# Kernel optimization log

Hardware: AMD Instinct MI355X
Metric: run time of the kernel (lower is better)

## Reference

```python
import jax, jax.numpy as jnp
import numpy as np

N = 50000          # num nodes
E = 800000         # edges per adjacency (avg degree 16)
NFEAT = 512
NHID = 256
NCLS = 100
LN_EPS = 1e-5


def spmm(rows, cols, vals, feat):
    # sparse [N,N] @ dense [N,F] via gather + segment-sum scatter
    return jax.ops.segment_sum(vals[:, None] * feat[cols], rows, num_segments=N)


def layernorm(h, g, b):
    mu = jnp.mean(h, axis=-1, keepdims=True)
    var = jnp.var(h, axis=-1, keepdims=True)
    return (h - mu) * jax.lax.rsqrt(var + LN_EPS) * g + b


def setup_inputs() -> dict:
    key = jax.random.key(0)
    ks = jax.random.split(key, 20)
    inp = {
        "x": jax.random.normal(ks[0], (N, NFEAT), dtype=jnp.float32),
        "adj_rows": jax.random.randint(ks[1], (4, E), 0, N, dtype=jnp.int32),
        "adj_cols": jax.random.randint(ks[2], (4, E), 0, N, dtype=jnp.int32),
        "adj_vals": jax.random.uniform(ks[3], (4, E), dtype=jnp.float32) / 16.0,
    }
    def lin(k, fin, fout):
        s = 1.0 / np.sqrt(fin)
        kw, kb = jax.random.split(k)
        return (jax.random.uniform(kw, (fin, fout), minval=-s, maxval=s, dtype=jnp.float32),
                jax.random.uniform(kb, (fout,), minval=-s, maxval=s, dtype=jnp.float32))
    # layer 0: GraphSage(nfeat -> nhid), LayerNorm over 2*nhid
    inp["W0"], inp["b0"] = lin(ks[4], NFEAT, NHID)
    inp["ln0_g"] = jnp.ones((2 * NHID,), jnp.float32)
    inp["ln0_b"] = jnp.zeros((2 * NHID,), jnp.float32)
    # layer 1: GCN(2*nhid -> nhid)
    inp["W1"], inp["b1"] = lin(ks[5], 2 * NHID, NHID)
    # layer 2: GraphSage(nhid -> nhid), LayerNorm over 2*nhid
    inp["W2"], inp["b2"] = lin(ks[6], NHID, NHID)
    inp["ln2_g"] = jnp.ones((2 * NHID,), jnp.float32)
    inp["ln2_b"] = jnp.zeros((2 * NHID,), jnp.float32)
    # layer 3: GCN(2*nhid -> nhid)
    inp["W3"], inp["b3"] = lin(ks[7], 2 * NHID, NHID)
    # output linear (nhid -> num_classes)
    inp["Wout"], inp["bout"] = lin(ks[8], NHID, NCLS)
    return inp


def reference(x, adj_rows, adj_cols, adj_vals,
              W0, b0, ln0_g, ln0_b, W1, b1, W2, b2, ln2_g, ln2_b, W3, b3,
              Wout, bout):
    # layer 0: GraphSage — feat = Linear(x); h = LN(concat([feat, A@feat])); ReLU; dropout(p=0)=id
    feat = x @ W0 + b0
    agg = spmm(adj_rows[0], adj_cols[0], adj_vals[0], feat)
    h = jax.nn.relu(layernorm(jnp.concatenate([feat, agg], axis=1), ln0_g, ln0_b))
    # layer 1: GCN — h = A @ Linear(h); ReLU
    h = jax.nn.relu(spmm(adj_rows[1], adj_cols[1], adj_vals[1], h @ W1 + b1))
    # layer 2: GraphSage
    feat = h @ W2 + b2
    agg = spmm(adj_rows[2], adj_cols[2], adj_vals[2], feat)
    h = jax.nn.relu(layernorm(jnp.concatenate([feat, agg], axis=1), ln2_g, ln2_b))
    # layer 3: GCN
    h = jax.nn.relu(spmm(adj_rows[3], adj_cols[3], adj_vals[3], h @ W3 + b3))
    # output head
    return h @ Wout + bout
```

## Files before the change

kernel.cpp:

```cpp
#include <hip/hip_runtime.h>

#define N_NODES 50000
#define E_EDGES 800000
#define NFEAT   512
#define NHID    256
#define NCLS    100
#define LN_EPS  1e-5f

#define NB     196
#define CHUNKA 6144
#define CAPB   6656

#define WT_TOTAL  (256*512 + 256*512 + 256*256 + 256*512 + 128*256)
#define XC_TOTAL  (N_NODES * NFEAT / 8)
#define PREP_TOTAL (WT_TOTAL + XC_TOTAL + 4 * NB)

typedef __attribute__((ext_vector_type(8))) short bf16x8;
typedef __attribute__((ext_vector_type(4))) float f32x4;

__device__ __forceinline__ ushort bf16_rne(float x) {
    unsigned u = __float_as_uint(x);
    unsigned r = u + 0x7FFFu + ((u >> 16) & 1u);
    return (ushort)(r >> 16);
}
__device__ __forceinline__ float bf16_to_f(ushort h) {
    return __uint_as_float(((unsigned)h) << 16);
}

__device__ __forceinline__ void gload16(const void* g, void* l) {
    __builtin_amdgcn_global_load_lds(
        (const __attribute__((address_space(1))) unsigned int*)g,
        (__attribute__((address_space(3))) unsigned int*)l, 16, 0, 0);
}

__global__ __launch_bounds__(256)
void prep_kernel(const float* __restrict__ W0, const float* __restrict__ W1,
                 const float* __restrict__ W2, const float* __restrict__ W3,
                 const float* __restrict__ Wo, const float* __restrict__ x,
                 ushort* __restrict__ W0T, ushort* __restrict__ W1T,
                 ushort* __restrict__ W2T, ushort* __restrict__ W3T,
                 ushort* __restrict__ WoT, ushort* __restrict__ Xb,
                 int* __restrict__ bcur)
{
    int idx = blockIdx.x * 256 + threadIdx.x;
    if (idx < WT_TOTAL) {
        const float* W; ushort* WT; int K, Nc;
        if      (idx < 131072) { W = W0; WT = W0T; K = 512; Nc = 256; }
        else if (idx < 262144) { idx -= 131072; W = W1; WT = W1T; K = 512; Nc = 256; }
        else if (idx < 327680) { idx -= 262144; W = W2; WT = W2T; K = 256; Nc = 256; }
        else if (idx < 458752) { idx -= 327680; W = W3; WT = W3T; K = 512; Nc = 256; }
        else                   { idx -= 458752; W = Wo; WT = WoT; K = 256; Nc = 100; }
        const int n = idx / K, k = idx - n * K;
        WT[idx] = bf16_rne((n < Nc) ? W[(size_t)k * Nc + n] : 0.f);
        return;
    }
    idx -= WT_TOTAL;
    if (idx < XC_TOTAL) {
        const float4 v0 = ((const float4*)x)[idx * 2];
        const float4 v1 = ((const float4*)x)[idx * 2 + 1];
        bf16x8 h;
        h[0] = (short)bf16_rne(v0.x); h[1] = (short)bf16_rne(v0.y);
        h[2] = (short)bf16_rne(v0.z); h[3] = (short)bf16_rne(v0.w);
        h[4] = (short)bf16_rne(v1.x); h[5] = (short)bf16_rne(v1.y);
        h[6] = (short)bf16_rne(v1.z); h[7] = (short)bf16_rne(v1.w);
        *(bf16x8*)&Xb[idx * 8] = h;
        return;
    }
    idx -= XC_TOTAL;
    if (idx < 4 * NB) bcur[idx] = 0;
}

template<int SWZ, int WF32, int WBF>
__global__ __launch_bounds__(512)
void gemm_mfma_bf16(const ushort* __restrict__ A1, const ushort* __restrict__ A2,
                    int K1, int K, const ushort* __restrict__ BT,
                    const float* __restrict__ bias, float* __restrict__ C,
                    ushort* __restrict__ Cbf, int M, int Nc)
{
    __shared__ __align__(16) ushort Ah[2][128 * 32];
    __shared__ __align__(16) ushort Bh[2][128 * 32];

    int bx, by;
    if (SWZ) {
        const int bid = blockIdx.x;
        const int g = bid >> 4;
        const int r = bid & 15;
        bx = g * 8 + (r & 7);
        by = r >> 3;
        if (bx >= (M + 127) / 128) return;
    } else {
        bx = blockIdx.x;
        by = blockIdx.y;
    }

    const int tid = threadIdx.x;
    const int bm  = bx * 128;
    const int bn  = by * 128;
    const int w   = tid >> 6;
    const int l   = tid & 63;
    const int wm  = (w >> 2) * 64;
    const int wn  = (w & 3) * 32;
    const int fr  = l & 15;
    const int fq  = l >> 4;

    const int gro = l >> 2;
    const int gch = ((l & 3) ^ (gro & 3)) * 8;
    const int ldsbase = (16 * w) * 32;

    f32x4 acc[4][2];
    #pragma unroll
    for (int i = 0; i < 4; ++i) {
        acc[i][0] = (f32x4){0.f, 0.f, 0.f, 0.f};
        acc[i][1] = (f32x4){0.f, 0.f, 0.f, 0.f};
    }

    const int K2 = K - K1;
    const int NS = K / 32;

    auto stage = [&](int s, int b) {
        const int k0 = s * 32;
        gload16(&BT[(size_t)(bn + 16 * w + gro) * K + k0 + gch], &Bh[b][ldsbase]);
        const ushort* asrc;
        if (k0 < K1) asrc = &A1[(size_t)(bm + 16 * w + gro) * K1 + k0 + gch];
        else         asrc = &A2[(size_t)(bm + 16 * w + gro) * K2 + (k0 - K1) + gch];
        gload16(asrc, &Ah[b][ldsbase]);
    };

    stage(0, 0);
    __syncthreads();

    int cur = 0;
    for (int s = 0; s < NS; ++s) {
        if (s + 1 < NS) stage(s + 1, cur ^ 1);

        bf16x8 bf[2];
        #pragma unroll
        for (int nf = 0; nf < 2; ++nf) {
            const int r = wn + nf * 16 + fr;
            bf[nf] = *(const bf16x8*)&Bh[cur][r * 32 + ((fq ^ (r & 3)) * 8)];
        }
        #pragma unroll
        for (int mf = 0; mf < 4; ++mf) {
            const int r = wm + mf * 16 + fr;
            const bf16x8 af = *(const bf16x8*)&Ah[cur][r * 32 + ((fq ^ (r & 3)) * 8)];
            acc[mf][0] = __builtin_amdgcn_mfma_f32_16x16x32_bf16(af, bf[0], acc[mf][0], 0, 0, 0);
            acc[mf][1] = __builtin_amdgcn_mfma_f32_16x16x32_bf16(af, bf[1], acc[mf][1], 0, 0, 0);
        }
        __syncthreads();
        cur ^= 1;
    }

    #pragma unroll
    for (int mf = 0; mf < 4; ++mf) {
        #pragma unroll
        for (int r = 0; r < 4; ++r) {
            const int row = bm + wm + mf * 16 + fq * 4 + r;
            if (row >= M) continue;
            #pragma unroll
            for (int nf = 0; nf < 2; ++nf) {
                const int col = bn + wn + nf * 16 + fr;
                if (col < Nc) {
                    const float v = acc[mf][nf][r] + bias[col];
                    if (WF32) C[(size_t)row * Nc + col] = v;
                    if (WBF)  Cbf[(size_t)row * Nc + col] = bf16_rne(v);
                }
            }
        }
    }
}

__global__ __launch_bounds__(256)
void bin_kernel(const int* __restrict__ rows, const int* __restrict__ cols,
                const float* __restrict__ vals, int* __restrict__ bcur,
                int2* __restrict__ est)
{
    __shared__ int cnt[NB];
    __shared__ int scn[256];
    __shared__ int cstart[NB];
    __shared__ int ccur[NB];
    __shared__ int garr[NB];
    __shared__ __align__(16) int2 buf[CHUNKA];

    const int a  = blockIdx.y;
    const int e0 = blockIdx.x * CHUNKA;
    const int n  = min(CHUNKA, E_EDGES - e0);
    const int t  = threadIdx.x;
    const int*   rp = rows + (size_t)a * E_EDGES + e0;
    const int*   cp = cols + (size_t)a * E_EDGES + e0;
    const float* vp = vals + (size_t)a * E_EDGES + e0;

    if (t < NB) cnt[t] = 0;
    __syncthreads();
    for (int i = t; i < n; i += 256) atomicAdd(&cnt[((unsigned)rp[i]) >> 8], 1);
    __syncthreads();

    scn[t] = (t < NB) ? cnt[t] : 0;
    __syncthreads();
    for (int off = 1; off < 256; off <<= 1) {
        const int v = (t >= off) ? scn[t - off] : 0;
        __syncthreads();
        scn[t] += v;
        __syncthreads();
    }
    if (t < NB) {
        const int ex = scn[t] - cnt[t];
        cstart[t] = ex;
        ccur[t]   = ex;
        garr[t]   = atomicAdd(&bcur[a * NB + t], cnt[t]);
    }
    __syncthreads();

    for (int i = t; i < n; i += 256) {
        const unsigned r = (unsigned)rp[i];
        const int b = r >> 8;
        const int p = atomicAdd(&ccur[b], 1);
        buf[p] = make_int2((int)((r << 16) | (unsigned)cp[i]), __float_as_int(vp[i]));
    }
    __syncthreads();

    for (int i = t; i < n; i += 256) {
        const int2 en = buf[i];
        const int b = ((unsigned)en.x) >> 24;
        const int slot = garr[b] + (i - cstart[b]);
        if (slot < CAPB)
            est[((size_t)(a * NB + b)) * CAPB + slot] = en;
    }
}

__global__ __launch_bounds__(256)
void sort_kernel(const int* __restrict__ bcur, const int2* __restrict__ est,
                 int2* __restrict__ cpk, int* __restrict__ rowstart)
{
    __shared__ __align__(16) int2 sbuf[CAPB];
    __shared__ __align__(16) int2 obuf[CAPB];
    __shared__ int cnt[256];
    __shared__ int scn[256];
    __shared__ int cur[256];

    const int a = blockIdx.y;
    const int b = blockIdx.x;
    const int t = threadIdx.x;
    const int nb = min(bcur[a * NB + b], CAPB);
    const int2* ei = est + ((size_t)(a * NB + b)) * CAPB;

    scn[t] = (t < b) ? bcur[a * NB + t] : 0;
    __syncthreads();
    for (int o = 128; o > 0; o >>= 1) {
        if (t < o) scn[t] += scn[t + o];
        __syncthreads();
    }
    const int bb = scn[0];
    __syncthreads();

    for (int i = t; i < nb; i += 256) sbuf[i] = ei[i];
    cnt[t] = 0;
    __syncthreads();
    for (int i = t; i < nb; i += 256)
        atomicAdd(&cnt[(((unsigned)sbuf[i].x) >> 16) & 255], 1);
    __syncthreads();

    scn[t] = cnt[t];
    __syncthreads();
    for (int off = 1; off < 256; off <<= 1) {
        const int v = (t >= off) ? scn[t - off] : 0;
        __syncthreads();
        scn[t] += v;
        __syncthreads();
    }
    const int excl = scn[t] - cnt[t];
    cur[t] = excl;

    const int r0 = b << 8;
    if (r0 + t < N_NODES)
        rowstart[(size_t)a * (N_NODES + 1) + r0 + t] = bb + excl;
    if (b == NB - 1 && t == 0)
        rowstart[(size_t)a * (N_NODES + 1) + N_NODES] = E_EDGES;
    __syncthreads();

    for (int i = t; i < nb; i += 256) {
        const int2 en = sbuf[i];
        const int r = (((unsigned)en.x) >> 16) & 255;
        const int p = atomicAdd(&cur[r], 1);
        obuf[p] = make_int2(en.x & 0xFFFF, en.y);
    }
    __syncthreads();

    int2* co = cpk + (size_t)a * E_EDGES + bb;
    for (int i = t; i < nb; i += 256) co[i] = obuf[i];
}

template<int LNFUSE>
__global__ __launch_bounds__(256)
void spmm_kernel(const int* __restrict__ rowstart, const int2* __restrict__ cpk,
                 const ushort* __restrict__ feat, ushort* __restrict__ out0,
                 ushort* __restrict__ out1, const float* __restrict__ g,
                 const float* __restrict__ be)
{
    const int row  = __builtin_amdgcn_readfirstlane((blockIdx.x * 256 + threadIdx.x) >> 6);
    const int lane = threadIdx.x & 63;

    const int s = __builtin_amdgcn_readfirstlane(rowstart[row]);
    const int e = __builtin_amdgcn_readfirstlane(rowstart[row + 1]);

    const ushort* fbase = feat + lane * 4;
    float ax = 0.f, ay = 0.f, az = 0.f, aw = 0.f;

    int j = s;
    for (; j + 16 <= e; j += 16) {
        #pragma unroll
        for (int q = 0; q < 16; ++q) {
            const int2 ev = cpk[j + q];
            const float v = __int_as_float(ev.y);
            const uint2 f = *(const uint2*)(fbase + (size_t)ev.x * NHID);
            ax += v * __uint_as_float(f.x << 16);
            ay += v * __uint_as_float(f.x & 0xFFFF0000u);
            az += v * __uint_as_float(f.y << 16);
            aw += v * __uint_as_float(f.y & 0xFFFF0000u);
        }
    }
    for (; j < e; ++j) {
        const int2 ev = cpk[j];
        const float v = __int_as_float(ev.y);
        const uint2 f = *(const uint2*)(fbase + (size_t)ev.x * NHID);
        ax += v * __uint_as_float(f.x << 16);
        ay += v * __uint_as_float(f.x & 0xFFFF0000u);
        az += v * __uint_as_float(f.y << 16);
        aw += v * __uint_as_float(f.y & 0xFFFF0000u);
    }

    if (LNFUSE) {
        const uint2 fx = *(const uint2*)(fbase + (size_t)row * NHID);
        float xf[4] = {__uint_as_float(fx.x << 16), __uint_as_float(fx.x & 0xFFFF0000u),
                       __uint_as_float(fx.y << 16), __uint_as_float(fx.y & 0xFFFF0000u)};

        float sum = xf[0] + xf[1] + xf[2] + xf[3] + ax + ay + az + aw;
        #pragma unroll
        for (int m = 1; m < 64; m <<= 1) sum += __shfl_xor(sum, m, 64);
        const float mean = sum * (1.f / 512.f);

        float sq = 0.f;
        #pragma unroll
        for (int jj = 0; jj < 4; ++jj) { const float d = xf[jj] - mean; sq += d * d; }
        { float d; d = ax - mean; sq += d * d; d = ay - mean; sq += d * d;
          d = az - mean; sq += d * d; d = aw - mean; sq += d * d; }
        #pragma unroll
        for (int m = 1; m < 64; m <<= 1) sq += __shfl_xor(sq, m, 64);
        const float rstd = rsqrtf(sq * (1.f / 512.f) + LN_EPS);

        const int col = lane * 4;
        const float av[4] = {ax, ay, az, aw};
        ushort4 o0, o1;
        float t0[4], t1[4];
        #pragma unroll
        for (int jj = 0; jj < 4; ++jj) {
            t0[jj] = fmaxf((xf[jj] - mean) * rstd * g[col + jj] + be[col + jj], 0.f);
            t1[jj] = fmaxf((av[jj] - mean) * rstd * g[256 + col + jj] + be[256 + col + jj], 0.f);
        }
        o0.x = bf16_rne(t0[0]); o0.y = bf16_rne(t0[1]); o0.z = bf16_rne(t0[2]); o0.w = bf16_rne(t0[3]);
        o1.x = bf16_rne(t1[0]); o1.y = bf16_rne(t1[1]); o1.z = bf16_rne(t1[2]); o1.w = bf16_rne(t1[3]);
        *(ushort4*)&out0[(size_t)row * NHID + col] = o0;
        *(ushort4*)&out1[(size_t)row * NHID + col] = o1;
    } else {
        ushort4 o;
        o.x = bf16_rne(fmaxf(ax, 0.f)); o.y = bf16_rne(fmaxf(ay, 0.f));
        o.z = bf16_rne(fmaxf(az, 0.f)); o.w = bf16_rne(fmaxf(aw, 0.f));
        *(ushort4*)&out0[(size_t)row * NHID + lane * 4] = o;
    }
}

extern "C" void kernel_launch(void* const* d_in, const int* in_sizes, int n_in,
                              void* d_out, int out_size, void* d_ws, size_t ws_size,
                              hipStream_t stream)
{
    const float* x    = (const float*)d_in[0];
    const int*   rows = (const int*)  d_in[1];
    const int*   cols = (const int*)  d_in[2];
    const float* vals = (const float*)d_in[3];
    const float* W0   = (const float*)d_in[4];
    const float* b0   = (const float*)d_in[5];
    const float* g0   = (const float*)d_in[6];
    const float* be0  = (const float*)d_in[7];
    const float* W1   = (const float*)d_in[8];
    const float* b1   = (const float*)d_in[9];
    const float* W2   = (const float*)d_in[10];
    const float* b2   = (const float*)d_in[11];
    const float* g2   = (const float*)d_in[12];
    const float* be2  = (const float*)d_in[13];
    const float* W3   = (const float*)d_in[14];
    const float* b3   = (const float*)d_in[15];
    const float* Wout = (const float*)d_in[16];
    const float* bout = (const float*)d_in[17];
    float* out = (float*)d_out;

    char* wsb = (char*)d_ws;
    size_t off = 0;
    auto carve = [&](size_t bytes) { void* p = wsb + off; off += (bytes + 255) & ~(size_t)255; return p; };
    int*    rowstart = (int*)   carve((size_t)4 * (N_NODES + 1) * 4);
    int*    bcur     = (int*)   carve((size_t)4 * NB * 4);
    int2*   cpk      = (int2*)  carve((size_t)4 * E_EDGES * 8);
    int2*   est      = (int2*)  carve((size_t)4 * NB * CAPB * 8);
    ushort* Xb       = (ushort*)carve((size_t)N_NODES * NFEAT * 2);
    ushort* F        = (ushort*)carve((size_t)N_NODES * NHID * 2);
    ushort* P        = (ushort*)carve((size_t)N_NODES * NHID * 2);
    ushort* Q        = (ushort*)carve((size_t)N_NODES * NHID * 2);
    ushort* G        = (ushort*)carve((size_t)N_NODES * NHID * 2);
    ushort* H        = (ushort*)carve((size_t)N_NODES * NHID * 2);
    ushort* W0T = (ushort*)carve((size_t)256 * 512 * 2);
    ushort* W1T = (ushort*)carve((size_t)256 * 512 * 2);
    ushort* W2T = (ushort*)carve((size_t)256 * 256 * 2);
    ushort* W3T = (ushort*)carve((size_t)256 * 512 * 2);
    ushort* WoT = (ushort*)carve((size_t)128 * 256 * 2);
    carve(131072);

    const dim3 blk(256);
    const dim3 blkg(512);
    const dim3 g_gemm(784);
    const dim3 g_head(391, 1);
    const dim3 g_bin((E_EDGES + CHUNKA - 1) / CHUNKA, 4);
    const dim3 g_sort(NB, 4);
    const int  row_blocks  = (N_NODES * 64 + 255) / 256;
    const int  prep_blocks = (PREP_TOTAL + 255) / 256;

    prep_kernel<<<prep_blocks, blk, 0, stream>>>(W0, W1, W2, W3, Wout, x,
                                                 W0T, W1T, W2T, W3T, WoT, Xb, bcur);
    bin_kernel<<<g_bin, blk, 0, stream>>>(rows, cols, vals, bcur, est);
    sort_kernel<<<g_sort, blk, 0, stream>>>(bcur, est, cpk, rowstart);

    const int* rs0 = rowstart;
    const int* rs1 = rowstart + (N_NODES + 1);
    const int* rs2 = rowstart + 2 * (N_NODES + 1);
    const int* rs3 = rowstart + 3 * (N_NODES + 1);
    const int2* c0 = cpk;
    const int2* c1 = cpk + E_EDGES;
    const int2* c2 = cpk + 2 * (size_t)E_EDGES;
    const int2* c3 = cpk + 3 * (size_t)E_EDGES;

    gemm_mfma_bf16<1,0,1><<<g_gemm, blkg, 0, stream>>>(Xb, Xb, 512, 512, W0T, b0, nullptr, F, N_NODES, 256);
    spmm_kernel<1><<<row_blocks, blk, 0, stream>>>(rs0, c0, F, P, Q, g0, be0);

    gemm_mfma_bf16<1,0,1><<<g_gemm, blkg, 0, stream>>>(P, Q, 256, 512, W1T, b1, nullptr, G, N_NODES, 256);
    spmm_kernel<0><<<row_blocks, blk, 0, stream>>>(rs1, c1, G, H, nullptr, nullptr, nullptr);

    gemm_mfma_bf16<1,0,1><<<g_gemm, blkg, 0, stream>>>(H, H, 256, 256, W2T, b2, nullptr, F, N_NODES, 256);
    spmm_kernel<1><<<row_blocks, blk, 0, stream>>>(rs2, c2, F, P, Q, g2, be2);

    gemm_mfma_bf16<1,0,1><<<g_gemm, blkg, 0, stream>>>(P, Q, 256, 512, W3T, b3, nullptr, G, N_NODES, 256);
    spmm_kernel<0><<<row_blocks, blk, 0, stream>>>(rs3, c3, G, H, nullptr, nullptr, nullptr);

    gemm_mfma_bf16<0,1,0><<<g_head, blkg, 0, stream>>>(H, H, 256, 256, WoT, bout, out, nullptr, N_NODES, 100);
}
```

Measured before the change: 471.2 us.

## Split SpMM into column-sliced row-group kernel and separate LayerNorm pass

Replaces the one-wave-per-row SpMM with a column-sliced kernel. Each 8-lane group handles one row for a 32-column slice, and eight slice blocks cover the 256 columns. The goal is more parallelism and smaller per-edge gathers that may fit cache behaviour better. The LayerNorm and ReLU that were fused into the SpMM epilogue move to a separate ln_pair_bf16 kernel. This adds an extra write and read of the aggregated features, re-reads the edge lists eight times, puts rows of different degree inside one wave, and drops the 16-way unrolled gather loop.

```diff
diff --git a/kernel.cpp b/kernel.cpp
--- a/kernel.cpp
+++ b/kernel.cpp
@@ -289,83 +289,93 @@
     for (int i = t; i < nb; i += 256) co[i] = obuf[i];
 }
 
-template<int LNFUSE>
+template<int RELU>
 __global__ __launch_bounds__(256)
-void spmm_kernel(const int* __restrict__ rowstart, const int2* __restrict__ cpk,
-                 const ushort* __restrict__ feat, ushort* __restrict__ out0,
-                 ushort* __restrict__ out1, const float* __restrict__ g,
-                 const float* __restrict__ be)
-{
-    const int row  = __builtin_amdgcn_readfirstlane((blockIdx.x * 256 + threadIdx.x) >> 6);
-    const int lane = threadIdx.x & 63;
-
-    const int s = __builtin_amdgcn_readfirstlane(rowstart[row]);
-    const int e = __builtin_amdgcn_readfirstlane(rowstart[row + 1]);
-
-    const ushort* fbase = feat + lane * 4;
+void spmm_slice(const int* __restrict__ rowstart, const int2* __restrict__ cpk,
+                const ushort* __restrict__ feat, ushort* __restrict__ out)
+{
+    const int bid   = blockIdx.x;
+    const int slice = bid & 7;
+    const int rblk  = bid >> 3;
+    const int t     = threadIdx.x;
+    const int w     = t >> 6;
+    const int lane  = t & 63;
+    const int grp   = lane >> 3;
+    const int l8    = lane & 7;
+
+    const int row = rblk * 32 + w * 8 + grp;
+    if (row >= N_NODES) return;
+
+    const int s = rowstart[row];
+    const int e = rowstart[row + 1];
+
+    const ushort* fb = feat + slice * 32 + l8 * 4;
     float ax = 0.f, ay = 0.f, az = 0.f, aw = 0.f;
 
-    int j = s;
-    for (; j + 16 <= e; j += 16) {
-        #pragma unroll
-        for (int q = 0; q < 16; ++q) {
-            const int2 ev = cpk[j + q];
-            const float v = __int_as_float(ev.y);
-            const uint2 f = *(const uint2*)(fbase + (size_t)ev.x * NHID);
-            ax += v * __uint_as_float(f.x << 16);
-            ay += v * __uint_as_float(f.x & 0xFFFF0000u);
-            az += v * __uint_as_float(f.y << 16);
-            aw += v * __uint_as_float(f.y & 0xFFFF0000u);
-        }
-    }
-    for (; j < e; ++j) {
+    for (int j = s; j < e; ++j) {
         const int2 ev = cpk[j];
         const float v = __int_as_float(ev.y);
-        const uint2 f = *(const uint2*)(fbase + (size_t)ev.x * NHID);
+        const uint2 f = *(const uint2*)(fb + (size_t)ev.x * NHID);
         ax += v * __uint_as_float(f.x << 16);
         ay += v * __uint_as_float(f.x & 0xFFFF0000u);
         az += v * __uint_as_float(f.y << 16);
         aw += v * __uint_as_float(f.y & 0xFFFF0000u);
     }
 
-    if (LNFUSE) {
-        const uint2 fx = *(const uint2*)(fbase + (size_t)row * NHID);
-        float xf[4] = {__uint_as_float(fx.x << 16), __uint_as_float(fx.x & 0xFFFF0000u),
-                       __uint_as_float(fx.y << 16), __uint_as_float(fx.y & 0xFFFF0000u)};
-
-        float sum = xf[0] + xf[1] + xf[2] + xf[3] + ax + ay + az + aw;
-        #pragma unroll
-        for (int m = 1; m < 64; m <<= 1) sum += __shfl_xor(sum, m, 64);
-        const float mean = sum * (1.f / 512.f);
-
-        float sq = 0.f;
-        #pragma unroll
-        for (int jj = 0; jj < 4; ++jj) { const float d = xf[jj] - mean; sq += d * d; }
-        { float d; d = ax - mean; sq += d * d; d = ay - mean; sq += d * d;
-          d = az - mean; sq += d * d; d = aw - mean; sq += d * d; }
-        #pragma unroll
-        for (int m = 1; m < 64; m <<= 1) sq += __shfl_xor(sq, m, 64);
-        const float rstd = rsqrtf(sq * (1.f / 512.f) + LN_EPS);
-
-        const int col = lane * 4;
-        const float av[4] = {ax, ay, az, aw};
-        ushort4 o0, o1;
-        float t0[4], t1[4];
-        #pragma unroll
-        for (int jj = 0; jj < 4; ++jj) {
-            t0[jj] = fmaxf((xf[jj] - mean) * rstd * g[col + jj] + be[col + jj], 0.f);
-            t1[jj] = fmaxf((av[jj] - mean) * rstd * g[256 + col + jj] + be[256 + col + jj], 0.f);
-        }
-        o0.x = bf16_rne(t0[0]); o0.y = bf16_rne(t0[1]); o0.z = bf16_rne(t0[2]); o0.w = bf16_rne(t0[3]);
-        o1.x = bf16_rne(t1[0]); o1.y = bf16_rne(t1[1]); o1.z = bf16_rne(t1[2]); o1.w = bf16_rne(t1[3]);
-        *(ushort4*)&out0[(size_t)row * NHID + col] = o0;
-        *(ushort4*)&out1[(size_t)row * NHID + col] = o1;
-    } else {
-        ushort4 o;
-        o.x = bf16_rne(fmaxf(ax, 0.f)); o.y = bf16_rne(fmaxf(ay, 0.f));
-        o.z = bf16_rne(fmaxf(az, 0.f)); o.w = bf16_rne(fmaxf(aw, 0.f));
-        *(ushort4*)&out0[(size_t)row * NHID + lane * 4] = o;
-    }
+    if (RELU) {
+        ax = fmaxf(ax, 0.f); ay = fmaxf(ay, 0.f);
+        az = fmaxf(az, 0.f); aw = fmaxf(aw, 0.f);
+    }
+    ushort4 o;
+    o.x = bf16_rne(ax); o.y = bf16_rne(ay);
+    o.z = bf16_rne(az); o.w = bf16_rne(aw);
+    *(ushort4*)&out[(size_t)row * NHID + slice * 32 + l8 * 4] = o;
+}
+
+__global__ __launch_bounds__(256)
+void ln_pair_bf16(const ushort* __restrict__ F, const ushort* __restrict__ AGG,
+                  const float* __restrict__ g, const float* __restrict__ be,
+                  ushort* __restrict__ P, ushort* __restrict__ Q)
+{
+    const int gid  = blockIdx.x * 256 + threadIdx.x;
+    const int row  = gid >> 6;
+    const int lane = gid & 63;
+    if (row >= N_NODES) return;
+
+    const ushort* src = (lane < 32) ? &F[(size_t)row * NHID + lane * 8]
+                                    : &AGG[(size_t)row * NHID + (lane - 32) * 8];
+    ushort* dst = (lane < 32) ? &P[(size_t)row * NHID + lane * 8]
+                              : &Q[(size_t)row * NHID + (lane - 32) * 8];
+
+    const ushort4 a0 = ((const ushort4*)src)[0];
+    const ushort4 a1 = ((const ushort4*)src)[1];
+    float x[8] = {bf16_to_f(a0.x), bf16_to_f(a0.y), bf16_to_f(a0.z), bf16_to_f(a0.w),
+                  bf16_to_f(a1.x), bf16_to_f(a1.y), bf16_to_f(a1.z), bf16_to_f(a1.w)};
+
+    float s = 0.f;
+    #pragma unroll
+    for (int j = 0; j < 8; ++j) s += x[j];
+    #pragma unroll
+    for (int m = 1; m < 64; m <<= 1) s += __shfl_xor(s, m, 64);
+    const float mean = s * (1.f / 512.f);
+
+    float sq = 0.f;
+    #pragma unroll
+    for (int j = 0; j < 8; ++j) { const float d = x[j] - mean; sq += d * d; }
+    #pragma unroll
+    for (int m = 1; m < 64; m <<= 1) sq += __shfl_xor(sq, m, 64);
+    const float rstd = rsqrtf(sq * (1.f / 512.f) + LN_EPS);
+
+    const int fb = lane * 8;
+    float o[8];
+    #pragma unroll
+    for (int j = 0; j < 8; ++j)
+        o[j] = fmaxf((x[j] - mean) * rstd * g[fb + j] + be[fb + j], 0.f);
+    ushort4 o0, o1;
+    o0.x = bf16_rne(o[0]); o0.y = bf16_rne(o[1]); o0.z = bf16_rne(o[2]); o0.w = bf16_rne(o[3]);
+    o1.x = bf16_rne(o[4]); o1.y = bf16_rne(o[5]); o1.z = bf16_rne(o[6]); o1.w = bf16_rne(o[7]);
+    ((ushort4*)dst)[0] = o0;
+    ((ushort4*)dst)[1] = o1;
 }
 
 extern "C" void kernel_launch(void* const* d_in, const int* in_sizes, int n_in,
@@ -418,6 +428,7 @@
     const dim3 g_head(391, 1);
     const dim3 g_bin((E_EDGES + CHUNKA - 1) / CHUNKA, 4);
     const dim3 g_sort(NB, 4);
+    const dim3 g_spmm(((N_NODES + 31) / 32) * 8);
     const int  row_blocks  = (N_NODES * 64 + 255) / 256;
     const int  prep_blocks = (PREP_TOTAL + 255) / 256;
 
@@ -436,16 +447,18 @@
     const int2* c3 = cpk + 3 * (size_t)E_EDGES;
 
     gemm_mfma_bf16<1,0,1><<<g_gemm, blkg, 0, stream>>>(Xb, Xb, 512, 512, W0T, b0, nullptr, F, N_NODES, 256);
-    spmm_kernel<1><<<row_blocks, blk, 0, stream>>>(rs0, c0, F, P, Q, g0, be0);
+    spmm_slice<0><<<g_spmm, blk, 0, stream>>>(rs0, c0, F, G);
+    ln_pair_bf16<<<row_blocks, blk, 0, stream>>>(F, G, g0, be0, P, Q);
 
     gemm_mfma_bf16<1,0,1><<<g_gemm, blkg, 0, stream>>>(P, Q, 256, 512, W1T, b1, nullptr, G, N_NODES, 256);
-    spmm_kernel<0><<<row_blocks, blk, 0, stream>>>(rs1, c1, G, H, nullptr, nullptr, nullptr);
+    spmm_slice<1><<<g_spmm, blk, 0, stream>>>(rs1, c1, G, H);
 
     gemm_mfma_bf16<1,0,1><<<g_gemm, blkg, 0, stream>>>(H, H, 256, 256, W2T, b2, nullptr, F, N_NODES, 256);
-    spmm_kernel<1><<<row_blocks, blk, 0, stream>>>(rs2, c2, F, P, Q, g2, be2);
+    spmm_slice<0><<<g_spmm, blk, 0, stream>>>(rs2, c2, F, G);
+    ln_pair_bf16<<<row_blocks, blk, 0, stream>>>(F, G, g2, be2, P, Q);
 
     gemm_mfma_bf16<1,0,1><<<g_gemm, blkg, 0, stream>>>(P, Q, 256, 512, W3T, b3, nullptr, G, N_NODES, 256);
-    spmm_kernel<0><<<row_blocks, blk, 0, stream>>>(rs3, c3, G, H, nullptr, nullptr, nullptr);
+    spmm_slice<1><<<g_spmm, blk, 0, stream>>>(rs3, c3, G, H);
 
     gemm_mfma_bf16<0,1,0><<<g_head, blkg, 0, stream>>>(H, H, 256, 256, WoT, bout, out, nullptr, N_NODES, 100);
 }
```

After: 733.0 us. 55.6% more time.
